# Performance work log

Hardware: AMD Instinct MI355X
Metric: run time of the kernel (lower is better)

Reference implementation:

```python
import math
import jax, jax.numpy as jnp
import numpy as np

LOG_NORM = -0.5 * math.log(2.0 * math.pi)  # per-dim gaussian normalizer
HEADS = 4
EM_ITERS = 5


def _mab(x, wq, bq, wk, bk, wv, bv, wo, bo):
    # Set-Transformer SAB(x) = MAB(x, x), ln=False
    B, S, D = x.shape
    dh = D // HEADS
    q = (x @ wq + bq).reshape(B, S, HEADS, dh)
    k = (x @ wk + bk).reshape(B, S, HEADS, dh)
    v = (x @ wv + bv).reshape(B, S, HEADS, dh)
    att = jax.nn.softmax(jnp.einsum('bqhd,bkhd->bhqk', q, k) / math.sqrt(D), axis=-1)
    o = q + jnp.einsum('bhqk,bkhd->bqhd', att, v)
    o = o.reshape(B, S, D)
    return o + jax.nn.relu(o @ wo + bo)


def setup_inputs() -> dict:
    key = jax.random.key(0)
    ks = jax.random.split(key, 16)
    B, S, D, L, K, MC = 16, 256, 512, 64, 20, 10
    s512 = 1.0 / math.sqrt(512.0)
    inp = {
        'H': jax.random.normal(ks[0], (B, S, D), jnp.float32),
        'eps': jax.random.normal(ks[1], (B * S, MC, L), jnp.float32),
        'sab_wq': jax.random.normal(ks[2], (2, D, D), jnp.float32) * s512,
        'sab_bq': jnp.zeros((2, D), jnp.float32),
        'sab_wk': jax.random.normal(ks[3], (2, D, D), jnp.float32) * s512,
        'sab_bk': jnp.zeros((2, D), jnp.float32),
        'sab_wv': jax.random.normal(ks[4], (2, D, D), jnp.float32) * s512,
        'sab_bv': jnp.zeros((2, D), jnp.float32),
        'sab_wo': jax.random.normal(ks[5], (2, D, D), jnp.float32) * s512,
        'sab_bo': jnp.zeros((2, D), jnp.float32),
        'wz': jax.random.normal(ks[6], (D, 2 * L), jnp.float32) * 0.02,
        'bz': jnp.zeros((2 * L,), jnp.float32),
        'w1': jax.random.normal(ks[7], (L, 2 * D), jnp.float32) * (1.0 / math.sqrt(L)),
        'b1': jnp.zeros((2 * D,), jnp.float32),
        'w2': jax.random.normal(ks[8], (2 * D, 2 * D), jnp.float32) * (1.0 / math.sqrt(2 * D)),
        'b2': jnp.zeros((2 * D,), jnp.float32),
        'w3': jax.random.normal(ks[9], (2 * D, D), jnp.float32) * (1.0 / math.sqrt(2 * D)),
        'b3': jnp.zeros((D,), jnp.float32),
    }
    rng = np.random.default_rng(1)
    # component_size distinct indices into the S*MC latent samples, per batch
    inp['init_idx'] = jnp.asarray(
        np.stack([rng.permutation(S * MC)[:K] for _ in range(B)]).astype(np.int32))
    return inp


def reference(H, eps, init_idx, sab_wq, sab_bq, sab_wk, sab_bk, sab_wv, sab_bv,
              sab_wo, sab_bo, wz, bz, w1, b1, w2, b2, w3, b3):
    B, S, D = H.shape
    MC, L = eps.shape[1], eps.shape[2]
    K = init_idx.shape[1]

    # q(z|x): two SABs + linear head
    h = H
    for i in range(2):
        h = _mab(h, sab_wq[i], sab_bq[i], sab_wk[i], sab_bk[i],
                 sab_wv[i], sab_bv[i], sab_wo[i], sab_bo[i])
    stats = h @ wz + bz                                    # [B,S,2L]
    mean, logvar = stats[..., :L], stats[..., L:]
    std = jnp.exp(0.5 * logvar)
    z = mean.reshape(B * S, 1, L) + eps * std.reshape(B * S, 1, L)
    z = z.reshape(B, S, MC, L)
    all_z = z.reshape(B, S * MC, L)                        # [B,N,L]

    # unsupervised EM prior (unit-variance GMM); distances via expansion
    pi = jnp.full((B, K), 1.0 / K, dtype=H.dtype)
    mu = jnp.take_along_axis(all_z, init_idx[:, :, None], axis=1)  # [B,K,L]
    x2 = jnp.sum(all_z * all_z, axis=-1)                   # [B,N]
    for _ in range(EM_ITERS):
        m2 = jnp.sum(mu * mu, axis=-1)                     # [B,K]
        ll = (-0.5 * (x2[:, :, None] - 2.0 * jnp.einsum('bnd,bkd->bnk', all_z, mu)
                      + m2[:, None, :]) + L * LOG_NORM + jnp.log(pi)[:, None, :])
        post = jax.nn.softmax(ll, axis=-1)                 # [B,N,K]
        Nk = post.sum(axis=1)                              # [B,K]
        pi = Nk / Nk.sum(axis=-1, keepdims=True)
        mu = jnp.einsum('bnk,bnd->bkd', post, all_z) / Nk[:, :, None]
    pi = jax.lax.stop_gradient(pi)
    mu = jax.lax.stop_gradient(mu)

    # reconstruction
    zf = z.reshape(-1, L)
    hr = jax.nn.relu(zf @ w1 + b1)
    hr = jax.nn.relu(hr @ w2 + b2)
    hr = jax.nn.relu(hr @ w3 + b3)
    hr = hr.reshape(B, S, MC, D)
    rec_loss = jnp.sum((hr - H[:, :, None, :]) ** 2) / (B * S * MC)

    # KL
    log_qz = jnp.sum(-0.5 * (logvar[:, :, None, :]
                             + (z - mean[:, :, None, :]) ** 2 / jnp.exp(logvar)[:, :, None, :])
                     + LOG_NORM, axis=-1)                  # [B,S,MC]
    z2 = jnp.sum(z * z, axis=-1)                           # [B,S,MC]
    m2 = jnp.sum(mu * mu, axis=-1)                         # [B,K]
    ll = (-0.5 * (z2[..., None] - 2.0 * jnp.einsum('bsmd,bkd->bsmk', z, mu)
                  + m2[:, None, None, :]) + L * LOG_NORM + jnp.log(pi)[:, None, None, :])
    log_pz = jax.scipy.special.logsumexp(ll, axis=-1)      # [B,S,MC]
    kl_loss = jnp.mean(log_qz - log_pz)
    return rec_loss, kl_loss
```

## Files before the change

### kernel.cpp

```cpp
#include <hip/hip_runtime.h>
#include <hip/hip_bf16.h>
#include <math.h>


#define BATCH 16
#define SEQ 256
#define DIM 512
#define NH 4
#define DH 128
#define LD 64
#define KC 20
#define MC 10
#define NPTS 2560
#define BS_TOT 4096
#define NROWS 40960
#define LOG_NORM (-0.9189385332046727f)

typedef __attribute__((ext_vector_type(8))) short bf16x8;
typedef __attribute__((ext_vector_type(4))) float f32x4;
typedef __hip_bfloat16 bf;

__device__ inline float warpReduceSum(float v) {
    for (int o = 32; o > 0; o >>= 1) v += __shfl_down(v, o);
    return v;
}

__device__ inline void async_copy16(const bf* g, bf* l) {
    __builtin_amdgcn_global_load_lds(
        (const __attribute__((address_space(1))) unsigned int*)g,
        (__attribute__((address_space(3))) unsigned int*)l, 16, 0, 0);
}

__device__ inline void split_store(float x, bf* ph, bf* pl, long idx) {
    const bf h = __float2bfloat16(x);
    ph[idx] = h;
    pl[idx] = __float2bfloat16(x - __bfloat162float(h));
}

template<int MODE>
__global__ __launch_bounds__(256, 3)
void gemm3t(const bf* __restrict__ Ah, const bf* __restrict__ Al,
            const bf* __restrict__ Bh, const bf* __restrict__ Bl,
            int K, int lda, int ldb,
            const float* __restrict__ b0, const float* __restrict__ b1v,
            const float* __restrict__ b2v,
            float* __restrict__ outF,
            bf* __restrict__ P1h, bf* __restrict__ P1l,
            bf* __restrict__ P2h, bf* __restrict__ P2l,
            bf* __restrict__ P3h, bf* __restrict__ P3l,
            const bf* __restrict__ Rh, const bf* __restrict__ Rl)
{
    __shared__ __align__(16) char smem[49152];
    float* Xs = (float*)smem;

    const int t = threadIdx.x;
    const int m0 = blockIdx.y * 64, n0 = blockIdx.x * 128;
    const int w = t >> 6, lane = t & 63;
    const int wn = w * 32;
    const int fm = lane & 15, quad = lane >> 4, fk = quad * 8;
    const int srow = t >> 2, scol = (t & 3) * 8;

    f32x4 acc[4][2];
#pragma unroll
    for (int i = 0; i < 4; i++)
#pragma unroll
        for (int j = 0; j < 2; j++) acc[i][j] = (f32x4){0.f, 0.f, 0.f, 0.f};

    const int nk2 = K >> 6;
    for (int kk2 = 0; kk2 < nk2; kk2++) {
#pragma unroll
        for (int h = 0; h < 2; h++) {
            const int kk = kk2 * 2 + h;
            char* base = smem + h * 24576;
            bf* Ash = (bf*)base;
            bf* Asl = (bf*)(base + 4096);
            bf* Bsh = (bf*)(base + 8192);
            bf* Bsl = (bf*)(base + 16384);
            const long ao = (long)(m0 + srow) * lda + kk * 32 + scol;
            const long bo = (long)(n0 + srow) * ldb + kk * 32 + scol;
            async_copy16(Ah + ao, Ash + w * 512);
            async_copy16(Al + ao, Asl + w * 512);
            async_copy16(Bh + bo, Bsh + w * 512);
            async_copy16(Bh + bo + 64L * ldb, Bsh + 2048 + w * 512);
            async_copy16(Bl + bo, Bsl + w * 512);
            async_copy16(Bl + bo + 64L * ldb, Bsl + 2048 + w * 512);
        }
        __syncthreads();

#pragma unroll
        for (int h = 0; h < 2; h++) {
            char* base = smem + h * 24576;
            bf* Ash = (bf*)base;
            bf* Asl = (bf*)(base + 4096);
            bf* Bsh = (bf*)(base + 8192);
            bf* Bsl = (bf*)(base + 16384);
            bf16x8 afh[4], afl[4], bfh[2], bfl[2];
#pragma unroll
            for (int mi = 0; mi < 4; mi++) {
                afh[mi] = *(const bf16x8*)&Ash[(mi * 16 + fm) * 32 + fk];
                afl[mi] = *(const bf16x8*)&Asl[(mi * 16 + fm) * 32 + fk];
            }
#pragma unroll
            for (int ni = 0; ni < 2; ni++) {
                bfh[ni] = *(const bf16x8*)&Bsh[(wn + ni * 16 + fm) * 32 + fk];
                bfl[ni] = *(const bf16x8*)&Bsl[(wn + ni * 16 + fm) * 32 + fk];
            }
#pragma unroll
            for (int mi = 0; mi < 4; mi++)
#pragma unroll
                for (int ni = 0; ni < 2; ni++) {
                    acc[mi][ni] = __builtin_amdgcn_mfma_f32_16x16x32_bf16(
                        afh[mi], bfh[ni], acc[mi][ni], 0, 0, 0);
                    acc[mi][ni] = __builtin_amdgcn_mfma_f32_16x16x32_bf16(
                        afh[mi], bfl[ni], acc[mi][ni], 0, 0, 0);
                    acc[mi][ni] = __builtin_amdgcn_mfma_f32_16x16x32_bf16(
                        afl[mi], bfh[ni], acc[mi][ni], 0, 0, 0);
                }
        }
        __syncthreads();
    }

    const int rl = t >> 2;
    const int cc4 = (t & 3) * 16;

    for (int p = 0; p < 2; p++) {
        if ((w >> 1) == p) {
            const int cb = wn - p * 64;
#pragma unroll
            for (int mi = 0; mi < 4; mi++)
#pragma unroll
                for (int ni = 0; ni < 2; ni++) {
                    const int c = cb + ni * 16 + fm;
#pragma unroll
                    for (int r = 0; r < 4; r++)
                        Xs[(mi * 16 + quad * 4 + r) * 68 + c] = acc[mi][ni][r];
                }
        }
        __syncthreads();

        if (MODE == 0 && n0 >= 1024) {
            const int hh = (n0 >> 7) & 3;
            const int dd = p * 64 + rl;
            const int bb = m0 >> 8;
            const int sb = (m0 & 255) + cc4;
            const float bias = b2v[hh * 128 + dd];
            const long ob = (((long)(bb * NH + hh) * DH + dd) << 8) + sb;
#pragma unroll
            for (int j = 0; j < 2; j++) {
                bf16x8 vh, vl;
#pragma unroll
                for (int i = 0; i < 8; i++) {
                    const float x = Xs[(cc4 + j * 8 + i) * 68 + rl] + bias;
                    const bf h = __float2bfloat16(x);
                    vh[i] = *(const short*)&h;
                    const bf l = __float2bfloat16(x - __bfloat162float(h));
                    vl[i] = *(const short*)&l;
                }
                *(bf16x8*)&P3h[ob + j * 8] = vh;
                *(bf16x8*)&P3l[ob + j * 8] = vl;
            }
        } else {
            float xv[16];
#pragma unroll
            for (int i = 0; i < 4; i++)
                *(float4*)&xv[i * 4] = *(const float4*)&Xs[rl * 68 + cc4 + i * 4];

            if (MODE == 0) {
                const int which = n0 >> 9;
                const int colq = (n0 & 511) + p * 64 + cc4;
                const float* bias = which ? b1v : b0;
                bf* Ph = which ? P2h : P1h;
                bf* Pl = which ? P2l : P1l;
                const long ob = (long)(m0 + rl) * 512 + colq;
#pragma unroll
                for (int j = 0; j < 2; j++) {
                    bf16x8 vh, vl;
#pragma unroll
                    for (int i = 0; i < 8; i++) {
                        const float x = xv[j * 8 + i] + bias[colq + j * 8 + i];
                        const bf h = __float2bfloat16(x); vh[i] = *(const short*)&h;
                        const bf l = __float2bfloat16(x - __bfloat162float(h));
                        vl[i] = *(const short*)&l;
                    }
                    *(bf16x8*)&Ph[ob + j * 8] = vh;
                    *(bf16x8*)&Pl[ob + j * 8] = vl;
                }
            } else if (MODE == 3) {
                const int colg = n0 + p * 64 + cc4;
                const long ob = (long)(m0 + rl) * 512 + colg;
#pragma unroll
                for (int j = 0; j < 2; j++) {
                    const bf16x8 rh = *(const bf16x8*)&Rh[ob + j * 8];
                    const bf16x8 rv = *(const bf16x8*)&Rl[ob + j * 8];
                    bf16x8 vh, vl;
#pragma unroll
                    for (int i = 0; i < 8; i++) {
                        short sh = rh[i], sl = rv[i];
                        float x = fmaxf(xv[j * 8 + i] + b0[colg + j * 8 + i], 0.f)
                                + __bfloat162float(*(const bf*)&sh)
                                + __bfloat162float(*(const bf*)&sl);
                        const bf h = __float2bfloat16(x); vh[i] = *(const short*)&h;
                        const bf l = __float2bfloat16(x - __bfloat162float(h));
                        vl[i] = *(const short*)&l;
                    }
                    *(bf16x8*)&P1h[ob + j * 8] = vh;
                    *(bf16x8*)&P1l[ob + j * 8] = vl;
                }
            } else {
                const int colg = p * 64 + cc4;
                const long ob = (long)(m0 + rl) * 128 + colg;
#pragma unroll
                for (int i = 0; i < 4; i++) {
                    float4 v = *(float4*)&xv[i * 4];
                    v.x += b0[colg + i * 4 + 0];
                    v.y += b0[colg + i * 4 + 1];
                    v.z += b0[colg + i * 4 + 2];
                    v.w += b0[colg + i * 4 + 3];
                    *(float4*)&outF[ob + i * 4] = v;
                }
            }
        }
        __syncthreads();
    }
}

__global__ __launch_bounds__(256)
void attn_fused(const bf* __restrict__ qh, const bf* __restrict__ ql,
                const bf* __restrict__ kh, const bf* __restrict__ kl,
                const bf* __restrict__ vTh, const bf* __restrict__ vTl,
                bf* __restrict__ oh, bf* __restrict__ ol)
{
    __shared__ __align__(16) char smem[43008];
    bf* Qsh = (bf*)smem;            bf* Qsl = (bf*)(smem + 4096);
    bf* Ksh = (bf*)(smem + 8192);   bf* Ksl = (bf*)(smem + 24576);
    bf* Psh = (bf*)smem;            bf* Psl = (bf*)(smem + 4096);
    bf* Vsh = (bf*)(smem + 8192);   bf* Vsl = (bf*)(smem + 16384);
    float (*red)[4]  = (float(*)[4])(smem + 40960);
    float (*red2)[4] = (float(*)[4])(smem + 41984);

    const int t = threadIdx.x;
    const int z = blockIdx.y;
    const int m0 = blockIdx.x * 64;
    const int bb = z >> 2, hh = z & 3;
    const long hOff = (long)bb * 131072 + (long)hh * 128;
    const long vOff = (long)z * 32768;

    const int w = t >> 6, lane = t & 63;
    const int fm = lane & 15;
    const int quad = lane >> 4;
    const int fk = quad * 8;
    const int srow = t >> 2, scol = (t & 3) * 8;

    f32x4 acc[4][4];
#pragma unroll
    for (int i = 0; i < 4; i++)
#pragma unroll
        for (int j = 0; j < 4; j++) acc[i][j] = (f32x4){0.f, 0.f, 0.f, 0.f};

    for (int kk = 0; kk < 4; kk++) {
        const long ao = hOff + (long)(m0 + srow) * 512 + kk * 32 + scol;
        const long bo = hOff + (long)srow * 512 + kk * 32 + scol;
        async_copy16(qh + ao, Qsh + w * 512);
        async_copy16(ql + ao, Qsl + w * 512);
#pragma unroll
        for (int j = 0; j < 4; j++) {
            async_copy16(kh + bo + (long)j * 64 * 512, Ksh + w * 512 + j * 2048);
            async_copy16(kl + bo + (long)j * 64 * 512, Ksl + w * 512 + j * 2048);
        }
        __syncthreads();

        bf16x8 afh[4], afl[4];
#pragma unroll
        for (int mi = 0; mi < 4; mi++) {
            afh[mi] = *(const bf16x8*)&Qsh[(mi * 16 + fm) * 32 + fk];
            afl[mi] = *(const bf16x8*)&Qsl[(mi * 16 + fm) * 32 + fk];
        }
#pragma unroll
        for (int ni = 0; ni < 4; ni++) {
            const bf16x8 bh = *(const bf16x8*)&Ksh[(w * 64 + ni * 16 + fm) * 32 + fk];
            const bf16x8 bl = *(const bf16x8*)&Ksl[(w * 64 + ni * 16 + fm) * 32 + fk];
#pragma unroll
            for (int mi = 0; mi < 4; mi++) {
                acc[mi][ni] = __builtin_amdgcn_mfma_f32_16x16x32_bf16(
                    afh[mi], bh, acc[mi][ni], 0, 0, 0);
                acc[mi][ni] = __builtin_amdgcn_mfma_f32_16x16x32_bf16(
                    afh[mi], bl, acc[mi][ni], 0, 0, 0);
                acc[mi][ni] = __builtin_amdgcn_mfma_f32_16x16x32_bf16(
                    afl[mi], bh, acc[mi][ni], 0, 0, 0);
            }
        }
        __syncthreads();
    }

    const float alpha = 0.044194173824159216f;
#pragma unroll
    for (int mi = 0; mi < 4; mi++)
#pragma unroll
        for (int r = 0; r < 4; r++) {
            float m = -1e30f;
#pragma unroll
            for (int ni = 0; ni < 4; ni++) m = fmaxf(m, acc[mi][ni][r]);
            for (int o = 8; o > 0; o >>= 1) m = fmaxf(m, __shfl_xor(m, o));
            if (fm == 0) red[mi * 16 + quad * 4 + r][w] = m;
        }
    __syncthreads();
    float invr[4][4];
#pragma unroll
    for (int mi = 0; mi < 4; mi++)
#pragma unroll
        for (int r = 0; r < 4; r++) {
            const int rowl = mi * 16 + quad * 4 + r;
            const float mx = fmaxf(fmaxf(red[rowl][0], red[rowl][1]),
                                   fmaxf(red[rowl][2], red[rowl][3]));
            float s = 0.f;
#pragma unroll
            for (int ni = 0; ni < 4; ni++) {
                const float e = __expf((acc[mi][ni][r] - mx) * alpha);
                acc[mi][ni][r] = e;
                s += e;
            }
            for (int o = 8; o > 0; o >>= 1) s += __shfl_xor(s, o);
            if (fm == 0) red2[rowl][w] = s;
        }
    __syncthreads();
#pragma unroll
    for (int mi = 0; mi < 4; mi++)
#pragma unroll
        for (int r = 0; r < 4; r++) {
            const int rowl = mi * 16 + quad * 4 + r;
            invr[mi][r] = 1.f / (red2[rowl][0] + red2[rowl][1] + red2[rowl][2] + red2[rowl][3]);
        }

    f32x4 acc2[4][2];
#pragma unroll
    for (int i = 0; i < 4; i++)
#pragma unroll
        for (int j = 0; j < 2; j++) acc2[i][j] = (f32x4){0.f, 0.f, 0.f, 0.f};

    for (int kc = 0; kc < 8; kc++) {
        if (w == (kc >> 1)) {
            const int nib = (kc & 1) * 2;
#pragma unroll
            for (int mi = 0; mi < 4; mi++)
#pragma unroll
                for (int r = 0; r < 4; r++) {
                    const int row = mi * 16 + quad * 4 + r;
#pragma unroll
                    for (int j = 0; j < 2; j++) {
                        const float p = acc[mi][nib + j][r] * invr[mi][r];
                        const int cc = j * 16 + fm;
                        const bf h = __float2bfloat16(p);
                        Psh[row * 32 + cc] = h;
                        Psl[row * 32 + cc] = __float2bfloat16(p - __bfloat162float(h));
                    }
                }
        }
        const long vo = vOff + (long)srow * 256 + kc * 32 + scol;
        async_copy16(vTh + vo, Vsh + w * 512);
        async_copy16(vTh + vo + 64L * 256, Vsh + w * 512 + 2048);
        async_copy16(vTl + vo, Vsl + w * 512);
        async_copy16(vTl + vo + 64L * 256, Vsl + w * 512 + 2048);
        __syncthreads();

        bf16x8 pfh[4], pfl[4];
#pragma unroll
        for (int mi = 0; mi < 4; mi++) {
            pfh[mi] = *(const bf16x8*)&Psh[(mi * 16 + fm) * 32 + fk];
            pfl[mi] = *(const bf16x8*)&Psl[(mi * 16 + fm) * 32 + fk];
        }
#pragma unroll
        for (int ni = 0; ni < 2; ni++) {
            const bf16x8 vh = *(const bf16x8*)&Vsh[(w * 32 + ni * 16 + fm) * 32 + fk];
            const bf16x8 vl = *(const bf16x8*)&Vsl[(w * 32 + ni * 16 + fm) * 32 + fk];
#pragma unroll
            for (int mi = 0; mi < 4; mi++) {
                acc2[mi][ni] = __builtin_amdgcn_mfma_f32_16x16x32_bf16(
                    pfh[mi], vh, acc2[mi][ni], 0, 0, 0);
                acc2[mi][ni] = __builtin_amdgcn_mfma_f32_16x16x32_bf16(
                    pfh[mi], vl, acc2[mi][ni], 0, 0, 0);
                acc2[mi][ni] = __builtin_amdgcn_mfma_f32_16x16x32_bf16(
                    pfl[mi], vh, acc2[mi][ni], 0, 0, 0);
            }
        }
        __syncthreads();
    }

#pragma unroll
    for (int ni = 0; ni < 2; ni++) {
        const int col = hh * 128 + w * 32 + ni * 16 + fm;
#pragma unroll
        for (int mi = 0; mi < 4; mi++)
#pragma unroll
            for (int r = 0; r < 4; r++) {
                const int row = mi * 16 + quad * 4 + r;
                const long idx = (long)(bb * 256 + m0 + row) * 512 + col;
                const float x = acc2[mi][ni][r]
                    + __bfloat162float(qh[idx]) + __bfloat162float(ql[idx]);
                split_store(x, oh, ol, idx);
            }
    }
}

template<bool SQLOSS>
__global__ __launch_bounds__(256, 3)
void gemm_mfma(const bf* __restrict__ A, const bf* __restrict__ BT,
               bf* __restrict__ C,
               const float* __restrict__ bias,
               const float* __restrict__ Href,
               float* __restrict__ lossAcc,
               int K, int N)
{
    __shared__ __align__(16) char smem[32768];
    bf* Cs  = (bf*)smem;
    __shared__ float redS[4];

    const int t = threadIdx.x;
    const int flat = blockIdx.y * gridDim.x + blockIdx.x;
    const int lane8 = flat & 7;
    const int grp = flat >> 3;
    const int n_blk = grp % gridDim.x;
    const int m_blk = (grp / gridDim.x) * 8 + lane8;
    const int m0 = m_blk * 128, n0 = n_blk * 128;

    const int w = t >> 6, lane = t & 63;
    const int wm = (w >> 1) * 64, wn = (w & 1) * 64;
    const int fm = lane & 15;
    const int quad = lane >> 4;
    const int fk = quad * 8;
    const int srow = t >> 2, scol = (t & 3) * 8;

    f32x4 acc[4][4];
#pragma unroll
    for (int i = 0; i < 4; i++)
#pragma unroll
        for (int j = 0; j < 4; j++) acc[i][j] = (f32x4){0.f, 0.f, 0.f, 0.f};

    const int nk2 = K >> 6;
    for (int kt2 = 0; kt2 < nk2; kt2++) {
#pragma unroll
        for (int h = 0; h < 2; h++) {
            const int kt = kt2 * 2 + h;
            bf* Asg = (bf*)(smem + h * 16384);
            bf* Bsg = (bf*)(smem + h * 16384 + 8192);
            const bf* ga = A + (long)(m0 + srow) * K + kt * 32 + scol;
            const bf* gb = BT + (long)(n0 + srow) * K + kt * 32 + scol;
            async_copy16(ga, Asg + w * 512);
            async_copy16(ga + 64L * K, Asg + 2048 + w * 512);
            async_copy16(gb, Bsg + w * 512);
            async_copy16(gb + 64L * K, Bsg + 2048 + w * 512);
        }
        __syncthreads();

#pragma unroll
        for (int h = 0; h < 2; h++) {
            bf* Asg = (bf*)(smem + h * 16384);
            bf* Bsg = (bf*)(smem + h * 16384 + 8192);
            bf16x8 af[4], bfr[4];
#pragma unroll
            for (int mi = 0; mi < 4; mi++)
                af[mi] = *(const bf16x8*)&Asg[(wm + mi * 16 + fm) * 32 + fk];
#pragma unroll
            for (int ni = 0; ni < 4; ni++)
                bfr[ni] = *(const bf16x8*)&Bsg[(wn + ni * 16 + fm) * 32 + fk];
#pragma unroll
            for (int mi = 0; mi < 4; mi++)
#pragma unroll
                for (int ni = 0; ni < 4; ni++)
                    acc[mi][ni] = __builtin_amdgcn_mfma_f32_16x16x32_bf16(
                        af[mi], bfr[ni], acc[mi][ni], 0, 0, 0);
        }
        __syncthreads();
    }

    if (SQLOSS) {
        float lsum = 0.f;
#pragma unroll
        for (int ni = 0; ni < 4; ni++) {
            const int col = n0 + wn + ni * 16 + fm;
            const float b = bias[col];
#pragma unroll
            for (int mi = 0; mi < 4; mi++)
#pragma unroll
                for (int r = 0; r < 4; r++) {
                    const int row = m0 + wm + mi * 16 + quad * 4 + r;
                    const float x = fmaxf(acc[mi][ni][r] + b, 0.f);
                    const float d = x - Href[(long)(row / MC) * DIM + col];
                    lsum = fmaf(d, d, lsum);
                }
        }
        lsum = warpReduceSum(lsum);
        if (lane == 0) redS[w] = lsum;
        __syncthreads();
        if (t == 0) atomicAdd(lossAcc, redS[0] + redS[1] + redS[2] + redS[3]);
    } else {
        for (int hf = 0; hf < 2; hf++) {
            if ((w >> 1) == hf) {
#pragma unroll
                for (int ni = 0; ni < 4; ni++) {
                    const int c = wn + ni * 16 + fm;
                    const float bv = bias[n0 + c];
#pragma unroll
                    for (int mi = 0; mi < 4; mi++)
#pragma unroll
                        for (int r = 0; r < 4; r++) {
                            const float x = fmaxf(acc[mi][ni][r] + bv, 0.f);
                            Cs[(mi * 16 + quad * 4 + r) * 136 + c] = __float2bfloat16(x);
                        }
                }
            }
            __syncthreads();
            const int rl2 = t >> 2, cc2 = (t & 3) * 32;
            const long ob = (long)(m0 + hf * 64 + rl2) * N + n0 + cc2;
#pragma unroll
            for (int j = 0; j < 4; j++)
                *(bf16x8*)&C[ob + j * 8] = *(const bf16x8*)&Cs[rl2 * 136 + cc2 + j * 8];
            __syncthreads();
        }
    }
}

__global__ void conv_all(
    const float* __restrict__ H, bf* __restrict__ h0h, bf* __restrict__ h0l,
    const float* __restrict__ wq, const float* __restrict__ wk,
    const float* __restrict__ wv, const float* __restrict__ wo,
    bf* __restrict__ qkvTh0, bf* __restrict__ qkvTl0,
    bf* __restrict__ woTh0, bf* __restrict__ woTl0,
    bf* __restrict__ qkvTh1, bf* __restrict__ qkvTl1,
    bf* __restrict__ woTh1, bf* __restrict__ woTl1,
    const float* __restrict__ wz, bf* __restrict__ wzTh, bf* __restrict__ wzTl,
    const float* __restrict__ w1, bf* __restrict__ w1T,
    const float* __restrict__ w2, bf* __restrict__ w2T,
    const float* __restrict__ w3, bf* __restrict__ w3T,
    float* __restrict__ scal, float* __restrict__ msP, float* __restrict__ nkP)
{
    const int t = threadIdx.x;
    if (blockIdx.x == 0 && t < 16) scal[t] = 0.f;
    const int gidx = blockIdx.x * 256 + t;
    if (gidx < 2097152) {
        const float x = H[gidx];
        const bf h = __float2bfloat16(x);
        h0h[gidx] = h;
        h0l[gidx] = __float2bfloat16(x - __bfloat162float(h));
        return;
    }
    const int idx = gidx - 2097152;
    if (idx < 2097152) {
        const int layer = idx >> 20;
        const int seg = (idx >> 18) & 3;
        const int r = idx & 262143;
        const int k = r >> 9, n = r & 511;
        const float* src = ((seg == 0) ? wq : (seg == 1) ? wk : (seg == 2) ? wv : wo)
                           + (long)layer * 262144;
        const float x = src[r];
        const bf h = __float2bfloat16(x);
        const bf l = __float2bfloat16(x - __bfloat162float(h));
        if (seg < 3) {
            const long o = (long)(seg * 512 + n) * 512 + k;
            if (layer == 0) { qkvTh0[o] = h; qkvTl0[o] = l; }
            else            { qkvTh1[o] = h; qkvTl1[o] = l; }
        } else {
            const long o = (long)n * 512 + k;
            if (layer == 0) { woTh0[o] = h; woTl0[o] = l; }
            else            { woTh1[o] = h; woTl1[o] = l; }
        }
    } else if (idx < 2162688) {
        const int i = idx - 2097152;
        const int k = i >> 7, n = i & 127;
        const float x = wz[i];
        const bf h = __float2bfloat16(x);
        wzTh[(long)n * 512 + k] = h;
        wzTl[(long)n * 512 + k] = __float2bfloat16(x - __bfloat162float(h));
    } else if (idx < 2228224) {
        const int i = idx - 2162688;
        const int k = i >> 10, n = i & 1023;
        w1T[(long)n * 64 + k] = __float2bfloat16(w1[i]);
    } else if (idx < 3276800) {
        const int i = idx - 2228224;
        const int k = i >> 10, n = i & 1023;
        w2T[(long)n * 1024 + k] = __float2bfloat16(w2[i]);
    } else if (idx < 3801088) {
        const int i = idx - 3276800;
        const int k = i >> 9, n = i & 511;
        w3T[(long)n * 1024 + k] = __float2bfloat16(w3[i]);
    } else if (idx < 3903488) {
        msP[20480 + (idx - 3801088)] = 0.f;
    } else if (idx < 3905088) {
        nkP[320 + (idx - 3903488)] = 0.f;
    }
}

__global__ __launch_bounds__(256)
void zgen(const float* __restrict__ stats, const float* __restrict__ eps,
          float* __restrict__ z, bf* __restrict__ z16)
{
    const int idx = blockIdx.x * 256 + threadIdx.x;
    const int bs = idx / 160;
    const int r = idx % 160;
    const int l4 = r % 16;
    const float4 e = ((const float4*)eps)[idx];
    const float4 mn = ((const float4*)stats)[bs * 32 + l4];
    const float4 lv = ((const float4*)stats)[bs * 32 + 16 + l4];
    float4 zz;
    zz.x = fmaf(e.x, expf(0.5f * lv.x), mn.x);
    zz.y = fmaf(e.y, expf(0.5f * lv.y), mn.y);
    zz.z = fmaf(e.z, expf(0.5f * lv.z), mn.z);
    zz.w = fmaf(e.w, expf(0.5f * lv.w), mn.w);
    ((float4*)z)[idx] = zz;
    bf* zp = z16 + (long)idx * 4;
    zp[0] = __float2bfloat16(zz.x);
    zp[1] = __float2bfloat16(zz.y);
    zp[2] = __float2bfloat16(zz.z);
    zp[3] = __float2bfloat16(zz.w);
}

__global__ void em_init(const float* __restrict__ z, const int* __restrict__ init_idx,
                        float* __restrict__ ms0, float* __restrict__ nk0)
{
    const int b = blockIdx.x, t = threadIdx.x;
    for (int i = t; i < KC * LD; i += 256) {
        const int k = i >> 6, l = i & 63;
        const int idx = init_idx[b * KC + k];
        ms0[b * KC * LD + i] = z[((long)b * NPTS + idx) * LD + l];
    }
    if (t < KC) nk0[b * KC + t] = 1.f;
}

__global__ __launch_bounds__(256)
void em_step(const float* __restrict__ z,
             const float* __restrict__ msIn, const float* __restrict__ nkIn,
             float* __restrict__ msOut, float* __restrict__ nkOut)
{
    __shared__ float muS[KC][65];
    __shared__ float m2lp[KC];
    __shared__ float NkU[KC];
    __shared__ float postS[KC][256];
    __shared__ float NkS[KC];

    const int tile = blockIdx.x, b = blockIdx.y, t = threadIdx.x;
    const int lane = t & 63, w = t >> 6;

    if (t < KC) NkU[t] = nkIn[b * KC + t];
    __syncthreads();
    for (int i = t; i < KC * LD; i += 256)
        muS[i >> 6][i & 63] = msIn[b * KC * LD + i] / NkU[i >> 6];
    __syncthreads();
    if (t < KC) {
        float s = 0.f;
        for (int l = 0; l < LD; l++) { const float m = muS[t][l]; s = fmaf(m, m, s); }
        float sn = 0.f;
        for (int k = 0; k < KC; k++) sn += NkU[k];
        m2lp[t] = -0.5f * s + logf(NkU[t] / sn);
    }
    __syncthreads();

    const long n = (long)tile * 256 + t;
    const float* zr = &z[((long)b * NPTS + n) * LD];
    float acc[KC];
#pragma unroll
    for (int k = 0; k < KC; k++) acc[k] = 0.f;
#pragma unroll
    for (int l4 = 0; l4 < 16; l4++) {
        const float4 zv = ((const float4*)zr)[l4];
#pragma unroll
        for (int k = 0; k < KC; k++) {
            acc[k] = fmaf(zv.x, muS[k][l4 * 4 + 0], acc[k]);
            acc[k] = fmaf(zv.y, muS[k][l4 * 4 + 1], acc[k]);
            acc[k] = fmaf(zv.z, muS[k][l4 * 4 + 2], acc[k]);
            acc[k] = fmaf(zv.w, muS[k][l4 * 4 + 3], acc[k]);
        }
    }
    float mx = -1e30f;
    float llv[KC];
#pragma unroll
    for (int k = 0; k < KC; k++) { llv[k] = acc[k] + m2lp[k]; mx = fmaxf(mx, llv[k]); }
    float s = 0.f;
#pragma unroll
    for (int k = 0; k < KC; k++) { llv[k] = expf(llv[k] - mx); s += llv[k]; }
    const float inv = 1.f / s;
#pragma unroll
    for (int k = 0; k < KC; k++) postS[k][t] = llv[k] * inv;
    __syncthreads();

#pragma unroll
    for (int kk = 0; kk < 5; kk++) {
        const int k = w * 5 + kk;
        float p = postS[k][lane] + postS[k][lane + 64] + postS[k][lane + 128] + postS[k][lane + 192];
        p = warpReduceSum(p);
        if (lane == 0) NkS[k] = p;
    }
    __syncthreads();

    const float* zb = &z[((long)b * NPTS + (long)tile * 256) * LD];
#pragma unroll
    for (int j = 0; j < 5; j++) {
        const int o = t + j * 256;
        const int k = o >> 6, l = o & 63;
        float sacc = 0.f;
        for (int n2 = 0; n2 < 256; n2++)
            sacc = fmaf(postS[k][n2], zb[n2 * LD + l], sacc);
        atomicAdd(&msOut[b * KC * LD + o], sacc);
    }
    if (t < KC) atomicAdd(&nkOut[b * KC + t], NkS[t]);
}

__global__ __launch_bounds__(256)
void kl_kernel(const float* __restrict__ z, const float* __restrict__ stats,
               const float* __restrict__ eps,
               const float* __restrict__ msIn, const float* __restrict__ nkIn,
               float* __restrict__ klAcc)
{
    __shared__ float muS[KC][65];
    __shared__ float m2lp[KC];
    __shared__ float NkU[KC];
    __shared__ float redS[4];

    const int tile = blockIdx.x, b = blockIdx.y, t = threadIdx.x;

    if (t < KC) NkU[t] = nkIn[b * KC + t];
    __syncthreads();
    for (int i = t; i < KC * LD; i += 256)
        muS[i >> 6][i & 63] = msIn[b * KC * LD + i] / NkU[i >> 6];
    __syncthreads();
    if (t < KC) {
        float s = 0.f;
        for (int l = 0; l < LD; l++) { const float m = muS[t][l]; s = fmaf(m, m, s); }
        float sn = 0.f;
        for (int k = 0; k < KC; k++) sn += NkU[k];
        m2lp[t] = -0.5f * s + logf(NkU[t] / sn);
    }
    __syncthreads();

    const int n = tile * 256 + t;
    const int sidx = n / MC, m = n % MC;
    const long bs = (long)b * SEQ + sidx;
    const float* zr = &z[((long)b * NPTS + n) * LD];

    float acc[KC];
#pragma unroll
    for (int k = 0; k < KC; k++) acc[k] = 0.f;
    float x2 = 0.f;
#pragma unroll
    for (int l4 = 0; l4 < 16; l4++) {
        const float4 zv = ((const float4*)zr)[l4];
        x2 = fmaf(zv.x, zv.x, fmaf(zv.y, zv.y, fmaf(zv.z, zv.z, fmaf(zv.w, zv.w, x2))));
#pragma unroll
        for (int k = 0; k < KC; k++) {
            acc[k] = fmaf(zv.x, muS[k][l4 * 4 + 0], acc[k]);
            acc[k] = fmaf(zv.y, muS[k][l4 * 4 + 1], acc[k]);
            acc[k] = fmaf(zv.z, muS[k][l4 * 4 + 2], acc[k]);
            acc[k] = fmaf(zv.w, muS[k][l4 * 4 + 3], acc[k]);
        }
    }
    float mx = -1e30f;
    float llv[KC];
#pragma unroll
    for (int k = 0; k < KC; k++) { llv[k] = acc[k] + m2lp[k]; mx = fmaxf(mx, llv[k]); }
    float s = 0.f;
#pragma unroll
    for (int k = 0; k < KC; k++) s += expf(llv[k] - mx);
    const float log_pz = -0.5f * x2 + mx + logf(s) + LD * LOG_NORM;

    const float* lvr = &stats[bs * 128 + 64];
    const float* er = &eps[(bs * MC + m) * LD];
    float slv = 0.f, se2 = 0.f;
#pragma unroll
    for (int l4 = 0; l4 < 16; l4++) {
        const float4 lv = ((const float4*)lvr)[l4];
        slv += lv.x + lv.y + lv.z + lv.w;
        const float4 e = ((const float4*)er)[l4];
        se2 = fmaf(e.x, e.x, fmaf(e.y, e.y, fmaf(e.z, e.z, fmaf(e.w, e.w, se2))));
    }
    const float log_qz = -0.5f * (slv + se2) + LD * LOG_NORM;

    float v = log_qz - log_pz;
    v = warpReduceSum(v);
    if ((t & 63) == 0) redS[t >> 6] = v;
    __syncthreads();
    if (t == 0) atomicAdd(klAcc, redS[0] + redS[1] + redS[2] + redS[3]);
}

__global__ void finalize(const float* __restrict__ scal, float* __restrict__ out)
{
    if (threadIdx.x == 0) {
        out[0] = scal[0] * (1.f / (float)NROWS);
        out[1] = scal[1] * (1.f / (float)NROWS);
    }
}

extern "C" void kernel_launch(void* const* d_in, const int* in_sizes, int n_in,
                              void* d_out, int out_size, void* d_ws, size_t ws_size,
                              hipStream_t stream)
{
    const float* H   = (const float*)d_in[0];
    const float* eps = (const float*)d_in[1];
    const float* wq  = (const float*)d_in[2];
    const float* bq  = (const float*)d_in[3];
    const float* wk  = (const float*)d_in[4];
    const float* bk  = (const float*)d_in[5];
    const float* wv  = (const float*)d_in[6];
    const float* bv  = (const float*)d_in[7];
    const float* wo  = (const float*)d_in[8];
    const float* bo  = (const float*)d_in[9];
    const float* wz  = (const float*)d_in[10];
    const float* bz  = (const float*)d_in[11];
    const float* w1  = (const float*)d_in[12];
    const float* b1  = (const float*)d_in[13];
    const float* w2  = (const float*)d_in[14];
    const float* b2  = (const float*)d_in[15];
    const float* w3  = (const float*)d_in[16];
    const float* b3  = (const float*)d_in[17];
    const int* init_idx = (const int*)d_in[18];
    float* out = (float*)d_out;
    float* wsf = (float*)d_ws;

    const long o_scal  = 0;
    const long o_nk    = 1024;
    const long o_ms    = 4096;
    const long o_st    = 131072;
    const long o_zb    = 655360;
    const long o_z16   = 3276800;
    const long o_q     = 4587520;
    const long o_k     = 6684672;
    const long o_vT    = 8781824;
    const long o_o     = 10878976;
    const long o_h1    = 12976128;
    const long o_qkvT0 = 15073280;
    const long o_woT0  = 15859712;
    const long o_qkvT1 = 16121856;
    const long o_woT1  = 16908288;
    const long o_wzT   = 17170432;
    const long o_w1T   = 17235968;
    const long o_w2T   = 17268736;
    const long o_w3T   = 17793024;
    const long o_d1    = 18055168;
    const long o_d2    = 39026688;

    const long PL = (long)BS_TOT * DIM;
    bf* qh  = (bf*)(wsf + o_q);   bf* ql  = qh + PL;
    bf* kh  = (bf*)(wsf + o_k);   bf* kl_ = kh + PL;
    bf* vTh = (bf*)(wsf + o_vT);  bf* vTl = vTh + PL;
    bf* oh  = (bf*)(wsf + o_o);   bf* ol  = oh + PL;
    bf* h1h = (bf*)(wsf + o_h1);  bf* h1l = h1h + PL;
    bf* h2h = qh;                 bf* h2l = ql;
    bf* qkvTh0 = (bf*)(wsf + o_qkvT0); bf* qkvTl0 = qkvTh0 + 1536L * 512;
    bf* woTh0  = (bf*)(wsf + o_woT0);  bf* woTl0  = woTh0 + 512L * 512;
    bf* qkvTh1 = (bf*)(wsf + o_qkvT1); bf* qkvTl1 = qkvTh1 + 1536L * 512;
    bf* woTh1  = (bf*)(wsf + o_woT1);  bf* woTl1  = woTh1 + 512L * 512;
    bf* wzTh = (bf*)(wsf + o_wzT);     bf* wzTl = wzTh + 128L * 512;
    bf* w1T = (bf*)(wsf + o_w1T);
    bf* w2T = (bf*)(wsf + o_w2T);
    bf* w3T = (bf*)(wsf + o_w3T);
    bf* z16 = (bf*)(wsf + o_z16);
    bf* d1  = (bf*)(wsf + o_d1);
    bf* d2  = (bf*)(wsf + o_d2);
    float* st = wsf + o_st;
    float* zb = wsf + o_zb;
    float* scal = wsf + o_scal;
    float* msP = wsf + o_ms;
    float* nkP = wsf + o_nk;

    const dim3 blk(256);

    conv_all<<<23447, blk, 0, stream>>>(
        H, h1h, h1l,
        wq, wk, wv, wo,
        qkvTh0, qkvTl0, woTh0, woTl0,
        qkvTh1, qkvTl1, woTh1, woTl1,
        wz, wzTh, wzTl, w1, w1T, w2, w2T, w3, w3T,
        scal, msP, nkP);

    for (int i = 0; i < 2; i++) {
        const long boff = (long)i * DIM;
        bf* qkh = i ? qkvTh1 : qkvTh0;  bf* qkl = i ? qkvTl1 : qkvTl0;
        bf* wh  = i ? woTh1 : woTh0;    bf* wl  = i ? woTl1 : woTl0;

        gemm3t<0><<<dim3(12, 64), blk, 0, stream>>>(
            h1h, h1l, qkh, qkl, 512, 512, 512,
            bq + boff, bk + boff, bv + boff, nullptr,
            qh, ql, kh, kl_, vTh, vTl, nullptr, nullptr);
        attn_fused<<<dim3(4, 64), blk, 0, stream>>>(qh, ql, kh, kl_, vTh, vTl, oh, ol);
        bf* houth = (i == 0) ? h1h : h2h;
        bf* houtl = (i == 0) ? h1l : h2l;
        gemm3t<3><<<dim3(4, 64), blk, 0, stream>>>(
            oh, ol, wh, wl, 512, 512, 512,
            bo + boff, nullptr, nullptr, nullptr,
            houth, houtl, nullptr, nullptr, nullptr, nullptr, oh, ol);
    }

    gemm3t<4><<<dim3(1, 64), blk, 0, stream>>>(
        h2h, h2l, wzTh, wzTl, 512, 512, 512,
        bz, nullptr, nullptr, st,
        nullptr, nullptr, nullptr, nullptr, nullptr, nullptr, nullptr, nullptr);

    zgen<<<2560, blk, 0, stream>>>(st, eps, zb, z16);

    gemm_mfma<false><<<dim3(8, 320), blk, 0, stream>>>(
        z16, w1T, d1, b1, nullptr, nullptr, 64, 1024);
    gemm_mfma<false><<<dim3(8, 320), blk, 0, stream>>>(
        d1, w2T, d2, b2, nullptr, nullptr, 1024, 1024);
    gemm_mfma<true><<<dim3(4, 320), blk, 0, stream>>>(
        d2, w3T, nullptr, b3, H, scal + 0, 1024, 512);

    em_init<<<16, blk, 0, stream>>>(zb, init_idx, msP, nkP);
    for (int it = 0; it < 5; it++) {
        em_step<<<dim3(10, 16), blk, 0, stream>>>(
            zb,
            msP + (long)it * 16 * KC * LD, nkP + (long)it * 16 * KC,
            msP + (long)(it + 1) * 16 * KC * LD, nkP + (long)(it + 1) * 16 * KC);
    }
    kl_kernel<<<dim3(10, 16), blk, 0, stream>>>(
        zb, st, eps,
        msP + 5L * 16 * KC * LD, nkP + 5L * 16 * KC, scal + 1);

    finalize<<<1, 64, 0, stream>>>(scal, out);
}
```

Baseline: 758.5 us.

## Add 256x256-tile 8-phase pipelined MFMA GEMM for second decoder layer

Adds a new bf16 MFMA GEMM kernel with 256x256 output tiles, 512 threads, double-buffered async global-to-LDS staging interleaved across eight phases, swizzled LDS layout, s_setprio around MFMA bursts, and an XCD-aware block swizzle. It replaces the generic gemm_mfma call for the 40960x1024x1024 decoder layer, the largest GEMM in the pipeline. The aim is to overlap memory loads with matrix math and raise data reuse per tile. The large static LDS footprint (~132KB) and high register use limit occupancy, and the tail clamping of k-tiles issues redundant loads.

```diff
diff --git a/kernel.cpp b/kernel.cpp
--- a/kernel.cpp
+++ b/kernel.cpp
@@ -517,6 +517,191 @@
             __syncthreads();
         }
     }
+}
+
+__global__ __launch_bounds__(512, 2)
+void gemm_8ph(const bf* __restrict__ A, const bf* __restrict__ BT,
+              bf* __restrict__ C, const float* __restrict__ bias,
+              int K, int N)
+{
+    __shared__ __align__(16) char smem8[135168];
+    bf* lds = (bf*)smem8;
+
+    const int t = threadIdx.x;
+    const int w = t >> 6, lane = t & 63;
+    const int wr = w >> 2, wc = w & 3;
+    const int fm = lane & 15, quad = lane >> 4, fm7 = fm & 7;
+
+    const int NNB = N >> 8;
+    const int cpx = gridDim.x >> 3;
+    const int bid = blockIdx.x;
+    const int swz = (bid & 7) * cpx + (bid >> 3);
+    const int m0 = (swz / NNB) * 256;
+    const int n0 = (swz % NNB) * 256;
+
+#define OffA(b, h) ((b) * 16384 + (h) * 8192)
+#define OffB(b, h) (32768 + (b) * 16384 + (h) * 8192)
+
+    const int r8 = lane >> 3;
+    const int c8 = (lane & 7) ^ r8;
+    const long ldk = (long)K;
+    const bf* pA0 = A  + (long)(m0 + w * 16 + r8) * ldk + c8 * 8;
+    const bf* pA1 = pA0 + 128L * ldk;
+    const bf* pB0 = BT + (long)(n0 + w * 16 + r8) * ldk + c8 * 8;
+    const bf* pB1 = pB0 + 128L * ldk;
+
+#define STAGE(BASE, KT, OFF) do {                                        \
+        const bf* _g = (BASE) + (KT) * 64;                               \
+        async_copy16(_g, &lds[(OFF) + w * 1024]);                        \
+        async_copy16(_g + (ldk << 3), &lds[(OFF) + w * 1024 + 512]);     \
+    } while (0)
+
+    bf16x8 fa[4][2], fb0[2][2], fb1[2][2];
+    f32x4 acc[8][4];
+#pragma unroll
+    for (int i = 0; i < 8; i++)
+#pragma unroll
+        for (int j = 0; j < 4; j++) acc[i][j] = (f32x4){0.f, 0.f, 0.f, 0.f};
+
+#define READ_A(b, qm) do {                                               \
+        const bf* Ab = &lds[OffA(b, wr)];                                \
+        _Pragma("unroll")                                                \
+        for (int mi2 = 0; mi2 < 4; mi2++) {                              \
+            const int lr = (qm) * 64 + mi2 * 16 + fm;                    \
+            fa[mi2][0] = *(const bf16x8*)&Ab[lr * 64 + ((quad) ^ fm7) * 8];      \
+            fa[mi2][1] = *(const bf16x8*)&Ab[lr * 64 + ((4 + quad) ^ fm7) * 8];  \
+        }                                                                \
+    } while (0)
+
+#define READ_B(b, qn, FB) do {                                           \
+        const bf* Bb = &lds[OffB(b, wc >> 1)];                           \
+        _Pragma("unroll")                                                \
+        for (int ni2 = 0; ni2 < 2; ni2++) {                              \
+            const int lr = (wc & 1) * 64 + ((qn) * 2 + ni2) * 16 + fm;   \
+            FB[ni2][0] = *(const bf16x8*)&Bb[lr * 64 + ((quad) ^ fm7) * 8];      \
+            FB[ni2][1] = *(const bf16x8*)&Bb[lr * 64 + ((4 + quad) ^ fm7) * 8];  \
+        }                                                                \
+    } while (0)
+
+#define MFMA_Q(qm, qn, FB) do {                                          \
+        _Pragma("unroll")                                                \
+        for (int mi2 = 0; mi2 < 4; mi2++)                                \
+            _Pragma("unroll")                                            \
+            for (int ni2 = 0; ni2 < 2; ni2++) {                          \
+                acc[(qm) * 4 + mi2][(qn) * 2 + ni2] =                    \
+                    __builtin_amdgcn_mfma_f32_16x16x32_bf16(             \
+                        fa[mi2][0], FB[ni2][0],                          \
+                        acc[(qm) * 4 + mi2][(qn) * 2 + ni2], 0, 0, 0);   \
+                acc[(qm) * 4 + mi2][(qn) * 2 + ni2] =                    \
+                    __builtin_amdgcn_mfma_f32_16x16x32_bf16(             \
+                        fa[mi2][1], FB[ni2][1],                          \
+                        acc[(qm) * 4 + mi2][(qn) * 2 + ni2], 0, 0, 0);   \
+            }                                                            \
+    } while (0)
+
+#define BAR()  __builtin_amdgcn_s_barrier()
+#define LGKM() asm volatile("s_waitcnt lgkmcnt(0)" ::: "memory")
+#define VM4()  asm volatile("s_waitcnt vmcnt(4)" ::: "memory")
+#define PRIO1() __builtin_amdgcn_s_setprio(1)
+#define PRIO0() __builtin_amdgcn_s_setprio(0)
+
+    const int NKT = K >> 6;
+    const int NIT = NKT >> 1;
+
+    STAGE(pB0, 0, OffB(0, 0));
+    STAGE(pB1, 0, OffB(0, 1));
+    STAGE(pA0, 0, OffA(0, 0));
+    STAGE(pA1, 0, OffA(0, 1));
+    STAGE(pB0, 1, OffB(1, 0));
+    STAGE(pB1, 1, OffB(1, 1));
+    VM4();
+    BAR();
+
+    for (int it = 0; it < NIT; it++) {
+        const int t1 = 2 * it + 1;
+        const int t2 = (2 * it + 2 < NKT) ? 2 * it + 2 : NKT - 1;
+        const int t3 = (2 * it + 3 < NKT) ? 2 * it + 3 : NKT - 1;
+
+        READ_A(0, 0);
+        READ_B(0, 0, fb0);
+        STAGE(pA0, t1, OffA(1, 0));
+        BAR(); LGKM();
+        PRIO1(); MFMA_Q(0, 0, fb0); PRIO0();
+        BAR();
+        READ_B(0, 1, fb1);
+        STAGE(pA1, t1, OffA(1, 1));
+        BAR(); LGKM();
+        PRIO1(); MFMA_Q(0, 1, fb1); PRIO0();
+        BAR();
+        READ_A(0, 1);
+        STAGE(pB0, t2, OffB(0, 0));
+        BAR(); LGKM();
+        PRIO1(); MFMA_Q(1, 1, fb1); PRIO0();
+        BAR();
+        STAGE(pB1, t2, OffB(0, 1));
+        BAR(); LGKM();
+        PRIO1(); MFMA_Q(1, 0, fb0); PRIO0();
+        VM4();
+        BAR();
+        READ_A(1, 0);
+        READ_B(1, 0, fb0);
+        STAGE(pA0, t2, OffA(0, 0));
+        BAR(); LGKM();
+        PRIO1(); MFMA_Q(0, 0, fb0); PRIO0();
+        BAR();
+        READ_B(1, 1, fb1);
+        STAGE(pA1, t2, OffA(0, 1));
+        BAR(); LGKM();
+        PRIO1(); MFMA_Q(0, 1, fb1); PRIO0();
+        BAR();
+        READ_A(1, 1);
+        STAGE(pB0, t3, OffB(1, 0));
+        BAR(); LGKM();
+        PRIO1(); MFMA_Q(1, 1, fb1); PRIO0();
+        BAR();
+        STAGE(pB1, t3, OffB(1, 1));
+        BAR(); LGKM();
+        PRIO1(); MFMA_Q(1, 0, fb0); PRIO0();
+        VM4();
+        BAR();
+    }
+
+    __syncthreads();
+
+    bf* Cs = (bf*)smem8;
+#pragma unroll
+    for (int ni = 0; ni < 4; ni++) {
+        const int c = wc * 64 + ni * 16 + fm;
+        const float bv = bias[n0 + c];
+#pragma unroll
+        for (int mi = 0; mi < 8; mi++)
+#pragma unroll
+            for (int r = 0; r < 4; r++) {
+                const int row = wr * 128 + mi * 16 + quad * 4 + r;
+                Cs[row * 264 + c] = __float2bfloat16(fmaxf(acc[mi][ni][r] + bv, 0.f));
+            }
+    }
+    __syncthreads();
+
+    const int srow = t >> 1;
+    const int scb = (t & 1) * 128;
+    const long ob = (long)(m0 + srow) * N + n0 + scb;
+    const bf* src = &Cs[srow * 264 + scb];
+#pragma unroll
+    for (int j = 0; j < 16; j++)
+        *(bf16x8*)&C[ob + j * 8] = *(const bf16x8*)&src[j * 8];
+
+#undef OffA
+#undef OffB
+#undef STAGE
+#undef READ_A
+#undef READ_B
+#undef MFMA_Q
+#undef BAR
+#undef LGKM
+#undef VM4
+#undef PRIO1
+#undef PRIO0
 }
 
 __global__ void conv_all(
@@ -896,8 +1081,7 @@
 
     gemm_mfma<false><<<dim3(8, 320), blk, 0, stream>>>(
         z16, w1T, d1, b1, nullptr, nullptr, 64, 1024);
-    gemm_mfma<false><<<dim3(8, 320), blk, 0, stream>>>(
-        d1, w2T, d2, b2, nullptr, nullptr, 1024, 1024);
+    gemm_8ph<<<dim3(640), dim3(512), 0, stream>>>(d1, w2T, d2, b2, 1024, 1024);
     gemm_mfma<true><<<dim3(4, 320), blk, 0, stream>>>(
         d2, w3T, nullptr, b3, H, scal + 0, 1024, 512);
 
```

Result: faster. 685.2 us (-9.7%).
